# Kernel optimization log

Measured on AMD Instinct MI355X. Metric: run time of the kernel, lower is better.

Reference implementation:

```python
import jax, jax.numpy as jnp
import numpy as np

N = 8192
IN_F = 512
OUT_F = 64
NEG_INF = -9e15

def setup_inputs() -> dict:
    key = jax.random.key(0)
    k1, k2, k3, k4 = jax.random.split(key, 4)
    node_features = jax.random.normal(k1, (N, IN_F), dtype=jnp.float32)
    adjacency_matrix = jax.random.randint(k2, (N, N), 0, 2, dtype=jnp.int32)
    # Xavier-uniform-like init (gain 1.414), scale irrelevant for correctness
    w_bound = 1.414 * np.sqrt(6.0 / (IN_F + OUT_F))
    a_bound = 1.414 * np.sqrt(6.0 / (2 * OUT_F + 1))
    weight_matrix = jax.random.uniform(k3, (IN_F, OUT_F), minval=-w_bound, maxval=w_bound, dtype=jnp.float32)
    attention_vector = jax.random.uniform(k4, (2 * OUT_F, 1), minval=-a_bound, maxval=a_bound, dtype=jnp.float32)
    return {
        "node_features": node_features,
        "adjacency_matrix": adjacency_matrix,
        "weight_matrix": weight_matrix,
        "attention_vector": attention_vector,
    }

def reference(node_features, adjacency_matrix, weight_matrix, attention_vector):
    # h: [N, F] transformed features
    h = node_features @ weight_matrix
    # score[i, j] = h[i] . a_left + h[j] . a_right
    a_left = attention_vector[:OUT_F, 0]   # [F]
    a_right = attention_vector[OUT_F:, 0]  # [F]
    scores = (h @ a_left)[:, None] + (h @ a_right)[None, :]  # [N, N]
    # NOTE: source defines leaky_relu but never applies it in forward — faithful omission.
    masked = jnp.where(adjacency_matrix > 0, scores, NEG_INF)
    attn = jax.nn.softmax(masked, axis=1)  # [N, N]
    # dropout p=0 / inference: no-op
    out = attn @ h  # [N, F]
    return jax.nn.elu(out)  # concat=True path
```

## Files before the change

### kernel.cpp

```cpp
#include <hip/hip_runtime.h>
#include <hip/hip_bf16.h>
#include <cstdint>

#define NN      8192
#define OF      64
#define NPAD    80
#define HWROWS  160
#define KSPLIT  8
#define LDSTR   72

#define OFF_H   0
#define OFF_R   2097152
#define OFF_HW  2129920
#define OFF_P   4751360

typedef __attribute__((ext_vector_type(8))) short  s16x8;
typedef __attribute__((ext_vector_type(4))) float  f32x4;

__device__ __forceinline__ unsigned short f2bf(float f) {
  unsigned int u = __float_as_uint(f);
  unsigned int r = (u + 0x7FFFu + ((u >> 16) & 1u)) >> 16;
  return (unsigned short)r;
}
__device__ __forceinline__ float bf2f(unsigned short s) {
  return __uint_as_float(((unsigned int)s) << 16);
}

__global__ __launch_bounds__(256) void k1_h_r(const float* __restrict__ X,
                                              const float* __restrict__ W,
                                              const float* __restrict__ att,
                                              float* __restrict__ h,
                                              float* __restrict__ r) {
  __shared__ float xs[16 * 516];
  __shared__ float ws[64 * 68];
  int t = threadIdx.x;
  int rb = blockIdx.x * 16;

  {
    const float4* src = (const float4*)(X + (size_t)rb * 512);
#pragma unroll
    for (int s = 0; s < 8; ++s) {
      int lid = s * 256 + t;
      int row = lid >> 7, kseg = lid & 127;
      *(float4*)&xs[row * 516 + kseg * 4] = src[row * 128 + kseg];
    }
  }

  int row = t >> 4, tx = t & 15;
  float4 acc = {0.f, 0.f, 0.f, 0.f};
  for (int kc = 0; kc < 8; ++kc) {
    __syncthreads();
#pragma unroll
    for (int s = 0; s < 4; ++s) {
      int lid = s * 256 + t;
      int k = lid >> 4, cs = lid & 15;
      *(float4*)&ws[k * 68 + cs * 4] =
          *(const float4*)(W + (size_t)(kc * 64 + k) * 64 + cs * 4);
    }
    __syncthreads();
#pragma unroll 16
    for (int k = 0; k < 64; ++k) {
      float x = xs[row * 516 + kc * 64 + k];
      float4 w4 = *(const float4*)&ws[k * 68 + tx * 4];
      acc.x += x * w4.x; acc.y += x * w4.y;
      acc.z += x * w4.z; acc.w += x * w4.w;
    }
  }
  *(float4*)(h + (size_t)(rb + row) * 64 + tx * 4) = acc;

  float v = acc.x * att[64 + tx * 4]     + acc.y * att[64 + tx * 4 + 1] +
            acc.z * att[64 + tx * 4 + 2] + acc.w * att[64 + tx * 4 + 3];
#pragma unroll
  for (int off = 8; off > 0; off >>= 1) v += __shfl_down(v, off, 16);
  if (tx == 0) r[rb + row] = v;
}

__global__ __launch_bounds__(256) void k2_hw(const float* __restrict__ h,
                                             const float* __restrict__ r,
                                             unsigned short* __restrict__ HW) {
  int j = blockIdx.x * 256 + threadIdx.x;
  int m = blockIdx.y;
  float e = expf(r[j]);
  int n = (m < 80) ? m : m - 80;
  float v;
  if (n < 64)      v = e * h[j * 64 + n];
  else if (n == 64) v = e;
  else             v = 0.f;
  unsigned short hi = f2bf(v);
  unsigned short val = (m < 80) ? hi : f2bf(v - bf2f(hi));
  HW[(size_t)m * NN + j] = val;
}

__device__ __forceinline__ s16x8 cvt8(int4 a, int4 b) {
  s16x8 f;
  f[0] = a.x > 0 ? (short)0x3F80 : (short)0;
  f[1] = a.y > 0 ? (short)0x3F80 : (short)0;
  f[2] = a.z > 0 ? (short)0x3F80 : (short)0;
  f[3] = a.w > 0 ? (short)0x3F80 : (short)0;
  f[4] = b.x > 0 ? (short)0x3F80 : (short)0;
  f[5] = b.y > 0 ? (short)0x3F80 : (short)0;
  f[6] = b.z > 0 ? (short)0x3F80 : (short)0;
  f[7] = b.w > 0 ? (short)0x3F80 : (short)0;
  return f;
}

__global__ __launch_bounds__(256, 2) void k3_gat(const int* __restrict__ A,
                                                 const unsigned short* __restrict__ HW,
                                                 float* __restrict__ P) {
  __shared__ unsigned short tile[HWROWS * LDSTR];

  int t = threadIdx.x;
  int rowTile = blockIdx.x >> 3;
  int ksId    = blockIdx.x & 7;
  int lane = t & 63, w = t >> 6;
  int l15 = lane & 15, q = lane >> 4;
  int rowBase = rowTile * 128 + w * 32;

  const int* ar0 = A + (size_t)(rowBase + l15) * NN;
  const int* ar1 = A + (size_t)(rowBase + 16 + l15) * NN;

  f32x4 acc[2][5];
#pragma unroll
  for (int mt = 0; mt < 2; ++mt)
#pragma unroll
    for (int tt = 0; tt < 5; ++tt) acc[mt][tt] = 0.f;

  int nrow[5], sg[5];
#pragma unroll
  for (int s = 0; s < 5; ++s) {
    int lid = s * 256 + t;
    nrow[s] = lid >> 3;
    sg[s]   = lid & 7;
  }

  int kk = ksId * (NN / KSPLIT);
  for (int step = 0; step < (NN / KSPLIT) / 64; ++step, kk += 64) {
    uint4 sv[5];
#pragma unroll
    for (int s = 0; s < 5; ++s)
      sv[s] = *(const uint4*)(HW + (size_t)nrow[s] * NN + kk + sg[s] * 8);

    int4 a00 = *(const int4*)(ar0 + kk + q * 8);
    int4 a01 = *(const int4*)(ar0 + kk + q * 8 + 4);
    int4 a02 = *(const int4*)(ar0 + kk + 32 + q * 8);
    int4 a03 = *(const int4*)(ar0 + kk + 32 + q * 8 + 4);
    int4 a10 = *(const int4*)(ar1 + kk + q * 8);
    int4 a11 = *(const int4*)(ar1 + kk + q * 8 + 4);
    int4 a12 = *(const int4*)(ar1 + kk + 32 + q * 8);
    int4 a13 = *(const int4*)(ar1 + kk + 32 + q * 8 + 4);

#pragma unroll
    for (int s = 0; s < 5; ++s)
      *(uint4*)&tile[nrow[s] * LDSTR + sg[s] * 8] = sv[s];

    s16x8 af[2][2];
    af[0][0] = cvt8(a00, a01);
    af[0][1] = cvt8(a02, a03);
    af[1][0] = cvt8(a10, a11);
    af[1][1] = cvt8(a12, a13);

    __syncthreads();

#pragma unroll
    for (int ks = 0; ks < 2; ++ks) {
#pragma unroll
      for (int tt = 0; tt < 5; ++tt) {
        int boff = (tt * 16 + l15) * LDSTR + ks * 32 + q * 8;
        s16x8 bhi = *(const s16x8*)&tile[boff];
        s16x8 blo = *(const s16x8*)&tile[boff + 80 * LDSTR];
        acc[0][tt] = __builtin_amdgcn_mfma_f32_16x16x32_bf16(af[0][ks], bhi, acc[0][tt], 0, 0, 0);
        acc[1][tt] = __builtin_amdgcn_mfma_f32_16x16x32_bf16(af[1][ks], bhi, acc[1][tt], 0, 0, 0);
        acc[0][tt] = __builtin_amdgcn_mfma_f32_16x16x32_bf16(af[0][ks], blo, acc[0][tt], 0, 0, 0);
        acc[1][tt] = __builtin_amdgcn_mfma_f32_16x16x32_bf16(af[1][ks], blo, acc[1][tt], 0, 0, 0);
      }
    }
    __syncthreads();
  }

  float* Pp = P + (size_t)ksId * NN * NPAD;
#pragma unroll
  for (int mt = 0; mt < 2; ++mt) {
    int rb = rowBase + mt * 16 + q * 4;
#pragma unroll
    for (int tt = 0; tt < 5; ++tt) {
      int col = tt * 16 + l15;
#pragma unroll
      for (int rg = 0; rg < 4; ++rg)
        Pp[(size_t)(rb + rg) * NPAD + col] = acc[mt][tt][rg];
    }
  }
}

__global__ __launch_bounds__(256) void k4_fin(const float* __restrict__ P,
                                              float* __restrict__ out) {
  int g = blockIdx.x * 256 + threadIdx.x;
  int i = g >> 6, c = g & 63;
  float num = 0.f, S = 0.f;
#pragma unroll
  for (int ks = 0; ks < KSPLIT; ++ks) {
    const float* p = P + (size_t)ks * NN * NPAD + (size_t)i * NPAD;
    num += p[c];
    S   += p[64];
  }
  float x = num / S;
  out[g] = x > 0.f ? x : expm1f(x);
}

extern "C" void kernel_launch(void* const* d_in, const int* in_sizes, int n_in,
                              void* d_out, int out_size, void* d_ws, size_t ws_size,
                              hipStream_t stream) {
  const float* X  = (const float*)d_in[0];
  const int*   A  = (const int*)d_in[1];
  const float* W  = (const float*)d_in[2];
  const float* av = (const float*)d_in[3];
  float* out = (float*)d_out;

  char* ws = (char*)d_ws;
  float*          h  = (float*)(ws + OFF_H);
  float*          r  = (float*)(ws + OFF_R);
  unsigned short* HW = (unsigned short*)(ws + OFF_HW);
  float*          P  = (float*)(ws + OFF_P);

  k1_h_r<<<NN / 16, 256, 0, stream>>>(X, W, av, h, r);
  k2_hw<<<dim3(NN / 256, HWROWS), 256, 0, stream>>>(h, r, HW);
  k3_gat<<<64 * KSPLIT, 256, 0, stream>>>(A, HW, P);
  k4_fin<<<(size_t)NN * OF / 256, 256, 0, stream>>>(P, out);
}
```

Measured before the change: 426.4 us.

## Load HW operand fragments directly from global memory, drop LDS tile and barriers

The GAT aggregation kernel no longer stages the bf16 HW hi/lo matrix through shared memory. Each lane now loads its MFMA B fragments straight from global memory, which removes both __syncthreads per step. The adjacency-to-bf16 conversion also becomes a packed multiply trick instead of per-element selects, which assumes adjacency values are exactly 0 or 1. The cost is that every wave reads the full HW tile from global/L2, four times the traffic of the shared staging, and register pressure goes up.

Result: slower. 455.0 us (+6.7%).

```diff
diff --git a/kernel.cpp b/kernel.cpp
--- a/kernel.cpp
+++ b/kernel.cpp
@@ -7,7 +7,6 @@
 #define NPAD    80
 #define HWROWS  160
 #define KSPLIT  8
-#define LDSTR   72
 
 #define OFF_H   0
 #define OFF_R   2097152
@@ -92,23 +91,17 @@
 }
 
 __device__ __forceinline__ s16x8 cvt8(int4 a, int4 b) {
-  s16x8 f;
-  f[0] = a.x > 0 ? (short)0x3F80 : (short)0;
-  f[1] = a.y > 0 ? (short)0x3F80 : (short)0;
-  f[2] = a.z > 0 ? (short)0x3F80 : (short)0;
-  f[3] = a.w > 0 ? (short)0x3F80 : (short)0;
-  f[4] = b.x > 0 ? (short)0x3F80 : (short)0;
-  f[5] = b.y > 0 ? (short)0x3F80 : (short)0;
-  f[6] = b.z > 0 ? (short)0x3F80 : (short)0;
-  f[7] = b.w > 0 ? (short)0x3F80 : (short)0;
-  return f;
+  union { unsigned u[4]; s16x8 v; } rr;
+  rr.u[0] = (unsigned)(a.x | (a.y << 16)) * 0x3F80u;
+  rr.u[1] = (unsigned)(a.z | (a.w << 16)) * 0x3F80u;
+  rr.u[2] = (unsigned)(b.x | (b.y << 16)) * 0x3F80u;
+  rr.u[3] = (unsigned)(b.z | (b.w << 16)) * 0x3F80u;
+  return rr.v;
 }
 
 __global__ __launch_bounds__(256, 2) void k3_gat(const int* __restrict__ A,
                                                  const unsigned short* __restrict__ HW,
                                                  float* __restrict__ P) {
-  __shared__ unsigned short tile[HWROWS * LDSTR];
-
   int t = threadIdx.x;
   int rowTile = blockIdx.x >> 3;
   int ksId    = blockIdx.x & 7;
@@ -116,8 +109,16 @@
   int l15 = lane & 15, q = lane >> 4;
   int rowBase = rowTile * 128 + w * 32;
 
-  const int* ar0 = A + (size_t)(rowBase + l15) * NN;
-  const int* ar1 = A + (size_t)(rowBase + 16 + l15) * NN;
+  const int* ar0 = A + (size_t)(rowBase + l15) * NN + ksId * (NN / KSPLIT) + q * 8;
+  const int* ar1 = ar0 + (size_t)16 * NN;
+
+  const unsigned short* bph[5];
+  const unsigned short* bpl[5];
+#pragma unroll
+  for (int tt = 0; tt < 5; ++tt) {
+    bph[tt] = HW + (size_t)(tt * 16 + l15) * NN + ksId * (NN / KSPLIT) + q * 8;
+    bpl[tt] = bph[tt] + (size_t)80 * NN;
+  }
 
   f32x4 acc[2][5];
 #pragma unroll
@@ -125,33 +126,24 @@
 #pragma unroll
     for (int tt = 0; tt < 5; ++tt) acc[mt][tt] = 0.f;
 
-  int nrow[5], sg[5];
-#pragma unroll
-  for (int s = 0; s < 5; ++s) {
-    int lid = s * 256 + t;
-    nrow[s] = lid >> 3;
-    sg[s]   = lid & 7;
-  }
-
-  int kk = ksId * (NN / KSPLIT);
-  for (int step = 0; step < (NN / KSPLIT) / 64; ++step, kk += 64) {
-    uint4 sv[5];
-#pragma unroll
-    for (int s = 0; s < 5; ++s)
-      sv[s] = *(const uint4*)(HW + (size_t)nrow[s] * NN + kk + sg[s] * 8);
-
-    int4 a00 = *(const int4*)(ar0 + kk + q * 8);
-    int4 a01 = *(const int4*)(ar0 + kk + q * 8 + 4);
-    int4 a02 = *(const int4*)(ar0 + kk + 32 + q * 8);
-    int4 a03 = *(const int4*)(ar0 + kk + 32 + q * 8 + 4);
-    int4 a10 = *(const int4*)(ar1 + kk + q * 8);
-    int4 a11 = *(const int4*)(ar1 + kk + q * 8 + 4);
-    int4 a12 = *(const int4*)(ar1 + kk + 32 + q * 8);
-    int4 a13 = *(const int4*)(ar1 + kk + 32 + q * 8 + 4);
-
-#pragma unroll
-    for (int s = 0; s < 5; ++s)
-      *(uint4*)&tile[nrow[s] * LDSTR + sg[s] * 8] = sv[s];
+  for (int step = 0; step < (NN / KSPLIT) / 64; ++step) {
+    int4 a00 = *(const int4*)(ar0);
+    int4 a01 = *(const int4*)(ar0 + 4);
+    int4 a02 = *(const int4*)(ar0 + 32);
+    int4 a03 = *(const int4*)(ar0 + 36);
+    int4 a10 = *(const int4*)(ar1);
+    int4 a11 = *(const int4*)(ar1 + 4);
+    int4 a12 = *(const int4*)(ar1 + 32);
+    int4 a13 = *(const int4*)(ar1 + 36);
+
+    s16x8 bhi[2][5], blo[2][5];
+#pragma unroll
+    for (int ks = 0; ks < 2; ++ks)
+#pragma unroll
+      for (int tt = 0; tt < 5; ++tt) {
+        bhi[ks][tt] = *(const s16x8*)(bph[tt] + ks * 32);
+        blo[ks][tt] = *(const s16x8*)(bpl[tt] + ks * 32);
+      }
 
     s16x8 af[2][2];
     af[0][0] = cvt8(a00, a01);
@@ -159,22 +151,19 @@
     af[1][0] = cvt8(a10, a11);
     af[1][1] = cvt8(a12, a13);
 
-    __syncthreads();
-
-#pragma unroll
-    for (int ks = 0; ks < 2; ++ks) {
+#pragma unroll
+    for (int ks = 0; ks < 2; ++ks)
 #pragma unroll
       for (int tt = 0; tt < 5; ++tt) {
-        int boff = (tt * 16 + l15) * LDSTR + ks * 32 + q * 8;
-        s16x8 bhi = *(const s16x8*)&tile[boff];
-        s16x8 blo = *(const s16x8*)&tile[boff + 80 * LDSTR];
-        acc[0][tt] = __builtin_amdgcn_mfma_f32_16x16x32_bf16(af[0][ks], bhi, acc[0][tt], 0, 0, 0);
-        acc[1][tt] = __builtin_amdgcn_mfma_f32_16x16x32_bf16(af[1][ks], bhi, acc[1][tt], 0, 0, 0);
-        acc[0][tt] = __builtin_amdgcn_mfma_f32_16x16x32_bf16(af[0][ks], blo, acc[0][tt], 0, 0, 0);
-        acc[1][tt] = __builtin_amdgcn_mfma_f32_16x16x32_bf16(af[1][ks], blo, acc[1][tt], 0, 0, 0);
+        acc[0][tt] = __builtin_amdgcn_mfma_f32_16x16x32_bf16(af[0][ks], bhi[ks][tt], acc[0][tt], 0, 0, 0);
+        acc[1][tt] = __builtin_amdgcn_mfma_f32_16x16x32_bf16(af[1][ks], bhi[ks][tt], acc[1][tt], 0, 0, 0);
+        acc[0][tt] = __builtin_amdgcn_mfma_f32_16x16x32_bf16(af[0][ks], blo[ks][tt], acc[0][tt], 0, 0, 0);
+        acc[1][tt] = __builtin_amdgcn_mfma_f32_16x16x32_bf16(af[1][ks], blo[ks][tt], acc[1][tt], 0, 0, 0);
       }
-    }
-    __syncthreads();
+
+    ar0 += 64; ar1 += 64;
+#pragma unroll
+    for (int tt = 0; tt < 5; ++tt) { bph[tt] += 64; bpl[tt] += 64; }
   }
 
   float* Pp = P + (size_t)ksId * NN * NPAD;
```

## Fuse HW packing into projection kernel and halve GAT row tile

Applied to the files above, without the earlier changes.

Folds the exp-weighted bf16 hi/lo packing of h into the projection kernel, removing the separate k2 launch and the h/r intermediate buffers. The GAT kernel now gives each wave 16 rows instead of 32, with double the grid and higher occupancy bounds. The adjacency-to-bf16 mask conversion uses a packed multiply trick instead of per-element selects. This assumes adjacency values are exactly 0 or 1, and it increases HW tile reloads per row.

Measured after the change: 411.0 us. -3.6%, faster.

```diff
diff --git a/kernel.cpp b/kernel.cpp
--- a/kernel.cpp
+++ b/kernel.cpp
@@ -9,10 +9,8 @@
 #define KSPLIT  8
 #define LDSTR   72
 
-#define OFF_H   0
-#define OFF_R   2097152
-#define OFF_HW  2129920
-#define OFF_P   4751360
+#define OFF_HW  0
+#define OFF_P   2621440
 
 typedef __attribute__((ext_vector_type(8))) short  s16x8;
 typedef __attribute__((ext_vector_type(4))) float  f32x4;
@@ -26,11 +24,10 @@
   return __uint_as_float(((unsigned int)s) << 16);
 }
 
-__global__ __launch_bounds__(256) void k1_h_r(const float* __restrict__ X,
-                                              const float* __restrict__ W,
-                                              const float* __restrict__ att,
-                                              float* __restrict__ h,
-                                              float* __restrict__ r) {
+__global__ __launch_bounds__(256) void k1_hw(const float* __restrict__ X,
+                                             const float* __restrict__ W,
+                                             const float* __restrict__ att,
+                                             unsigned short* __restrict__ HW) {
   __shared__ float xs[16 * 516];
   __shared__ float ws[64 * 68];
   int t = threadIdx.x;
@@ -66,45 +63,43 @@
       acc.z += x * w4.z; acc.w += x * w4.w;
     }
   }
-  *(float4*)(h + (size_t)(rb + row) * 64 + tx * 4) = acc;
 
   float v = acc.x * att[64 + tx * 4]     + acc.y * att[64 + tx * 4 + 1] +
             acc.z * att[64 + tx * 4 + 2] + acc.w * att[64 + tx * 4 + 3];
 #pragma unroll
-  for (int off = 8; off > 0; off >>= 1) v += __shfl_down(v, off, 16);
-  if (tx == 0) r[rb + row] = v;
-}
-
-__global__ __launch_bounds__(256) void k2_hw(const float* __restrict__ h,
-                                             const float* __restrict__ r,
-                                             unsigned short* __restrict__ HW) {
-  int j = blockIdx.x * 256 + threadIdx.x;
-  int m = blockIdx.y;
-  float e = expf(r[j]);
-  int n = (m < 80) ? m : m - 80;
-  float v;
-  if (n < 64)      v = e * h[j * 64 + n];
-  else if (n == 64) v = e;
-  else             v = 0.f;
-  unsigned short hi = f2bf(v);
-  unsigned short val = (m < 80) ? hi : f2bf(v - bf2f(hi));
-  HW[(size_t)m * NN + j] = val;
+  for (int m = 8; m > 0; m >>= 1) v += __shfl_xor(v, m, 64);
+  float e = expf(v);
+
+  int j = rb + row;
+  unsigned short* hw = HW + j;
+  float hv[4] = {acc.x, acc.y, acc.z, acc.w};
+#pragma unroll
+  for (int c = 0; c < 4; ++c) {
+    float val = e * hv[c];
+    unsigned short hi = f2bf(val);
+    hw[(size_t)(tx * 4 + c) * NN]      = hi;
+    hw[(size_t)(80 + tx * 4 + c) * NN] = f2bf(val - bf2f(hi));
+  }
+  if (tx == 0) {
+    unsigned short ehi = f2bf(e);
+    hw[(size_t)64 * NN]  = ehi;
+    hw[(size_t)144 * NN] = f2bf(e - bf2f(ehi));
+  } else {
+    hw[(size_t)(64 + tx) * NN]  = 0;
+    hw[(size_t)(144 + tx) * NN] = 0;
+  }
 }
 
 __device__ __forceinline__ s16x8 cvt8(int4 a, int4 b) {
-  s16x8 f;
-  f[0] = a.x > 0 ? (short)0x3F80 : (short)0;
-  f[1] = a.y > 0 ? (short)0x3F80 : (short)0;
-  f[2] = a.z > 0 ? (short)0x3F80 : (short)0;
-  f[3] = a.w > 0 ? (short)0x3F80 : (short)0;
-  f[4] = b.x > 0 ? (short)0x3F80 : (short)0;
-  f[5] = b.y > 0 ? (short)0x3F80 : (short)0;
-  f[6] = b.z > 0 ? (short)0x3F80 : (short)0;
-  f[7] = b.w > 0 ? (short)0x3F80 : (short)0;
-  return f;
-}
-
-__global__ __launch_bounds__(256, 2) void k3_gat(const int* __restrict__ A,
+  union { unsigned u[4]; s16x8 v; } rr;
+  rr.u[0] = (unsigned)(a.x | (a.y << 16)) * 0x3F80u;
+  rr.u[1] = (unsigned)(a.z | (a.w << 16)) * 0x3F80u;
+  rr.u[2] = (unsigned)(b.x | (b.y << 16)) * 0x3F80u;
+  rr.u[3] = (unsigned)(b.z | (b.w << 16)) * 0x3F80u;
+  return rr.v;
+}
+
+__global__ __launch_bounds__(256, 4) void k3_gat(const int* __restrict__ A,
                                                  const unsigned short* __restrict__ HW,
                                                  float* __restrict__ P) {
   __shared__ unsigned short tile[HWROWS * LDSTR];
@@ -114,16 +109,13 @@
   int ksId    = blockIdx.x & 7;
   int lane = t & 63, w = t >> 6;
   int l15 = lane & 15, q = lane >> 4;
-  int rowBase = rowTile * 128 + w * 32;
-
-  const int* ar0 = A + (size_t)(rowBase + l15) * NN;
-  const int* ar1 = A + (size_t)(rowBase + 16 + l15) * NN;
-
-  f32x4 acc[2][5];
-#pragma unroll
-  for (int mt = 0; mt < 2; ++mt)
-#pragma unroll
-    for (int tt = 0; tt < 5; ++tt) acc[mt][tt] = 0.f;
+  int rowBase = rowTile * 64 + w * 16;
+
+  const int* ar0 = A + (size_t)(rowBase + l15) * NN + ksId * (NN / KSPLIT) + q * 8;
+
+  f32x4 acc[5];
+#pragma unroll
+  for (int tt = 0; tt < 5; ++tt) acc[tt] = 0.f;
 
   int nrow[5], sg[5];
 #pragma unroll
@@ -140,54 +132,43 @@
     for (int s = 0; s < 5; ++s)
       sv[s] = *(const uint4*)(HW + (size_t)nrow[s] * NN + kk + sg[s] * 8);
 
-    int4 a00 = *(const int4*)(ar0 + kk + q * 8);
-    int4 a01 = *(const int4*)(ar0 + kk + q * 8 + 4);
-    int4 a02 = *(const int4*)(ar0 + kk + 32 + q * 8);
-    int4 a03 = *(const int4*)(ar0 + kk + 32 + q * 8 + 4);
-    int4 a10 = *(const int4*)(ar1 + kk + q * 8);
-    int4 a11 = *(const int4*)(ar1 + kk + q * 8 + 4);
-    int4 a12 = *(const int4*)(ar1 + kk + 32 + q * 8);
-    int4 a13 = *(const int4*)(ar1 + kk + 32 + q * 8 + 4);
+    int4 a00 = *(const int4*)(ar0);
+    int4 a01 = *(const int4*)(ar0 + 4);
+    int4 a02 = *(const int4*)(ar0 + 32);
+    int4 a03 = *(const int4*)(ar0 + 36);
+    ar0 += 64;
 
 #pragma unroll
     for (int s = 0; s < 5; ++s)
       *(uint4*)&tile[nrow[s] * LDSTR + sg[s] * 8] = sv[s];
 
-    s16x8 af[2][2];
-    af[0][0] = cvt8(a00, a01);
-    af[0][1] = cvt8(a02, a03);
-    af[1][0] = cvt8(a10, a11);
-    af[1][1] = cvt8(a12, a13);
-
-    __syncthreads();
-
-#pragma unroll
-    for (int ks = 0; ks < 2; ++ks) {
+    s16x8 af[2];
+    af[0] = cvt8(a00, a01);
+    af[1] = cvt8(a02, a03);
+
+    __syncthreads();
+
+#pragma unroll
+    for (int ks = 0; ks < 2; ++ks)
 #pragma unroll
       for (int tt = 0; tt < 5; ++tt) {
         int boff = (tt * 16 + l15) * LDSTR + ks * 32 + q * 8;
         s16x8 bhi = *(const s16x8*)&tile[boff];
         s16x8 blo = *(const s16x8*)&tile[boff + 80 * LDSTR];
-        acc[0][tt] = __builtin_amdgcn_mfma_f32_16x16x32_bf16(af[0][ks], bhi, acc[0][tt], 0, 0, 0);
-        acc[1][tt] = __builtin_amdgcn_mfma_f32_16x16x32_bf16(af[1][ks], bhi, acc[1][tt], 0, 0, 0);
-        acc[0][tt] = __builtin_amdgcn_mfma_f32_16x16x32_bf16(af[0][ks], blo, acc[0][tt], 0, 0, 0);
-        acc[1][tt] = __builtin_amdgcn_mfma_f32_16x16x32_bf16(af[1][ks], blo, acc[1][tt], 0, 0, 0);
+        acc[tt] = __builtin_amdgcn_mfma_f32_16x16x32_bf16(af[ks], bhi, acc[tt], 0, 0, 0);
+        acc[tt] = __builtin_amdgcn_mfma_f32_16x16x32_bf16(af[ks], blo, acc[tt], 0, 0, 0);
       }
-    }
     __syncthreads();
   }
 
   float* Pp = P + (size_t)ksId * NN * NPAD;
-#pragma unroll
-  for (int mt = 0; mt < 2; ++mt) {
-    int rb = rowBase + mt * 16 + q * 4;
-#pragma unroll
-    for (int tt = 0; tt < 5; ++tt) {
-      int col = tt * 16 + l15;
-#pragma unroll
-      for (int rg = 0; rg < 4; ++rg)
-        Pp[(size_t)(rb + rg) * NPAD + col] = acc[mt][tt][rg];
-    }
+  int rb = rowBase + q * 4;
+#pragma unroll
+  for (int tt = 0; tt < 5; ++tt) {
+    int col = tt * 16 + l15;
+#pragma unroll
+    for (int rg = 0; rg < 4; ++rg)
+      Pp[(size_t)(rb + rg) * NPAD + col] = acc[tt][rg];
   }
 }
 
@@ -216,13 +197,10 @@
   float* out = (float*)d_out;
 
   char* ws = (char*)d_ws;
-  float*          h  = (float*)(ws + OFF_H);
-  float*          r  = (float*)(ws + OFF_R);
   unsigned short* HW = (unsigned short*)(ws + OFF_HW);
   float*          P  = (float*)(ws + OFF_P);
 
-  k1_h_r<<<NN / 16, 256, 0, stream>>>(X, W, av, h, r);
-  k2_hw<<<dim3(NN / 256, HWROWS), 256, 0, stream>>>(h, r, HW);
-  k3_gat<<<64 * KSPLIT, 256, 0, stream>>>(A, HW, P);
+  k1_hw<<<NN / 16, 256, 0, stream>>>(X, W, av, HW);
+  k3_gat<<<128 * KSPLIT, 256, 0, stream>>>(A, HW, P);
   k4_fin<<<(size_t)NN * OF / 256, 256, 0, stream>>>(P, out);
 }
```
